# Performance work log

Hardware: AMD Instinct MI355X
Metric: run time of the kernel (lower is better)

## Reference

```python
import jax, jax.numpy as jnp
import numpy as np

DECAY = 0.999
EPS = 1e-05
COMMIT = 0.25


def _layer_norm(x, g, b, eps=1e-5):
    mu = x.mean(-1, keepdims=True)
    var = ((x - mu) ** 2).mean(-1, keepdims=True)
    return (x - mu) * jax.lax.rsqrt(var + eps) * g + b


def setup_inputs() -> dict:
    key = jax.random.key(0)
    ks = jax.random.split(key, 8)
    B, T, D, M, H = 8, 4096, 512, 1024, 512
    init_bound = 1.0 / 512
    embedding = jax.random.uniform(ks[0], (M, D), jnp.float32, -init_bound, init_bound)
    return {
        "dense_x": jax.random.normal(ks[1], (B, T, D), jnp.float32),
        "dense_padding_mask": jax.random.randint(ks[2], (B, T), 0, 2).astype(bool),
        "labels": jax.random.randint(ks[3], (B, T), 0, M),
        "embedding": embedding,
        "ema_count": jnp.zeros((M,), jnp.float32),
        "ema_weight": embedding,
        "ln1_g": jnp.ones((D,), jnp.float32),
        "ln1_b": jnp.zeros((D,), jnp.float32),
        "W1": jax.random.normal(ks[4], (D, H), jnp.float32) * (1.0 / np.sqrt(D)),
        "ln2_g": jnp.ones((H,), jnp.float32),
        "ln2_b": jnp.zeros((H,), jnp.float32),
        "W2": jax.random.normal(ks[5], (H, M), jnp.float32) * (1.0 / np.sqrt(H)),
    }


def reference(dense_x, dense_padding_mask, labels, embedding, ema_count, ema_weight,
              ln1_g, ln1_b, W1, ln2_g, ln2_b, W2):
    B, T, D = dense_x.shape
    M = embedding.shape[0]
    N = B * T

    # ---- VQ codebook (EMA) ----
    x_flat = jax.lax.stop_gradient(dense_x).reshape(N, D)
    distances = (jnp.sum(embedding ** 2, axis=1)[None, :]
                 + jnp.sum(x_flat ** 2, axis=1, keepdims=True)
                 - 2.0 * (x_flat @ embedding.T))
    indices = jnp.argmin(distances, axis=-1)  # [N]
    quantized = embedding[indices].reshape(B, T, D)

    # EMA codebook update (training path); encodings.sum(0) and encodings.T @ x
    # expressed as scatter-adds instead of materializing [N, M] one-hot.
    counts = jnp.zeros((M,), dense_x.dtype).at[indices].add(1.0)
    new_count = DECAY * ema_count + (1.0 - DECAY) * counts
    n = jnp.sum(new_count)
    new_count = (new_count + EPS) / (n + M * EPS) * n
    dw = jnp.zeros((M, D), dense_x.dtype).at[indices].add(x_flat)
    new_weight = DECAY * ema_weight + (1.0 - DECAY) * dw
    new_embedding = new_weight / new_count[:, None]

    e_latent_loss = (dense_x - jax.lax.stop_gradient(quantized)) ** 2  # [B,T,D]
    vq_loss = COMMIT * e_latent_loss
    quantized_st = dense_x + jax.lax.stop_gradient(quantized - dense_x)

    avg_probs = counts / N
    perplexity = jnp.exp(-jnp.sum(avg_probs * jnp.log(avg_probs + 1e-10)))

    # ---- decoder: LN -> ReLU -> Linear -> LN -> ReLU -> Linear ----
    h = jax.nn.relu(_layer_norm(dense_x, ln1_g, ln1_b)) @ W1      # [B,T,H]
    logits = jax.nn.relu(_layer_norm(h, ln2_g, ln2_b)) @ W2       # [B,T,M]

    # ---- cross-entropy with ignore_index=-1 (padding) ----
    lab = jnp.where(dense_padding_mask, -1, labels)
    valid = lab >= 0
    safe = jnp.where(valid, lab, 0)
    logp = jax.nn.log_softmax(logits, axis=-1)
    ce = -jnp.take_along_axis(logp, safe[..., None], axis=-1)[..., 0]
    recon_loss = jnp.where(valid, ce, 0.0)

    loss = recon_loss + vq_loss.sum(-1)  # [B,T]
    return quantized_st, loss, perplexity, new_embedding, new_count, new_weight
```

## Files before the change

kernel.cpp:

```cpp
#include <hip/hip_runtime.h>


#define N_TOK 32768
#define WAITV(n) __builtin_amdgcn_s_waitcnt(0x0F70 | (n))
#define BAR() __builtin_amdgcn_s_barrier()

typedef __attribute__((ext_vector_type(8))) short short8;
typedef _Float16 half8 __attribute__((ext_vector_type(8)));
typedef __attribute__((ext_vector_type(4))) float f32x4;

__device__ __forceinline__ f32x4 mfma16(short8 a, short8 b, f32x4 c) {
    return __builtin_amdgcn_mfma_f32_16x16x32_bf16(a, b, c, 0, 0, 0);
}
__device__ __forceinline__ f32x4 mfma16h(half8 a, half8 b, f32x4 c) {
    return __builtin_amdgcn_mfma_f32_16x16x32_f16(a, b, c, 0, 0, 0);
}

__device__ __forceinline__ void gl_lds16(const unsigned short* g, char* l) {
    __builtin_amdgcn_global_load_lds(
        (const __attribute__((address_space(1))) void*)g,
        (__attribute__((address_space(3))) void*)l, 16, 0, 0);
}

__device__ __forceinline__ unsigned short f2bf(float x) {
    unsigned u = __float_as_uint(x);
    u += 0x7fffu + ((u >> 16) & 1u);
    return (unsigned short)(u >> 16);
}
__device__ __forceinline__ float bf2f(unsigned short h) {
    return __uint_as_float(((unsigned)h) << 16);
}
__device__ __forceinline__ unsigned short f2h(float x) {
    union { _Float16 h; unsigned short u; } c;
    c.h = (_Float16)x;
    return c.u;
}
__device__ __forceinline__ float h2f(unsigned short u) {
    union { _Float16 h; unsigned short u; } c;
    c.u = u;
    return (float)c.h;
}

__device__ __forceinline__ float waveSum(float v) {
#pragma unroll
    for (int off = 32; off > 0; off >>= 1) v += __shfl_down(v, off, 64);
    return v;
}
__device__ __forceinline__ float xorSum(float v) {
#pragma unroll
    for (int off = 1; off < 64; off <<= 1) v += __shfl_xor(v, off);
    return v;
}

__global__ __launch_bounds__(256) void prep_x_kernel(
        const float* __restrict__ X, const float* __restrict__ g,
        const float* __restrict__ b, unsigned short* __restrict__ Xf,
        unsigned short* __restrict__ A1, unsigned long long* __restrict__ minpack) {
    int tid = threadIdx.x;
    if (tid < 4) minpack[(blockIdx.x << 2) + tid] = ~0ULL;
    int lane = tid & 63;
    int n = (blockIdx.x << 2) + (tid >> 6);
    const float* row = X + ((size_t)n << 9);
    float v[8]; float s = 0.f, ss = 0.f;
#pragma unroll
    for (int i = 0; i < 8; ++i) { v[i] = row[lane + (i << 6)]; s += v[i]; ss += v[i] * v[i]; }
    s = xorSum(s); ss = xorSum(ss);
    float mu = s * (1.f / 512.f);
    float rs = rsqrtf(ss * (1.f / 512.f) - mu * mu + 1e-5f);
#pragma unroll
    for (int i = 0; i < 8; ++i) {
        int c = lane + (i << 6);
        size_t o = ((size_t)n << 9) + c;
        float x = v[i];
        Xf[o] = f2h(x);
        float a = fmaxf((x - mu) * rs * g[c] + b[c], 0.f);
        A1[o] = f2bf(a);
    }
}

__global__ __launch_bounds__(256) void prep_h_kernel(
        const unsigned short* __restrict__ Hb, const float* __restrict__ g,
        const float* __restrict__ b, unsigned short* __restrict__ A2) {
    int lane = threadIdx.x & 63;
    int n = (blockIdx.x << 2) + (threadIdx.x >> 6);
    const unsigned short* row = Hb + ((size_t)n << 9);
    float v[8]; float s = 0.f, ss = 0.f;
#pragma unroll
    for (int i = 0; i < 8; ++i) { v[i] = bf2f(row[lane + (i << 6)]); s += v[i]; ss += v[i] * v[i]; }
    s = xorSum(s); ss = xorSum(ss);
    float mu = s * (1.f / 512.f);
    float rs = rsqrtf(ss * (1.f / 512.f) - mu * mu + 1e-5f);
#pragma unroll
    for (int i = 0; i < 8; ++i) {
        int c = lane + (i << 6);
        float a = fmaxf((v[i] - mu) * rs * g[c] + b[c], 0.f);
        A2[((size_t)n << 9) + c] = f2bf(a);
    }
}

__global__ __launch_bounds__(256) void prep_e_kernel(
        const float* __restrict__ E, unsigned short* __restrict__ Ehf,
        unsigned short* __restrict__ Elf, float* __restrict__ e_sq,
        int* __restrict__ izero) {
    if (blockIdx.x < 8) izero[(blockIdx.x << 8) + threadIdx.x] = 0;
    int lane = threadIdx.x & 63;
    int m = (blockIdx.x << 2) + (threadIdx.x >> 6);
    const float* row = E + ((size_t)m << 9);
    float ss = 0.f;
#pragma unroll
    for (int i = 0; i < 8; ++i) {
        int c = lane + (i << 6);
        float x = row[c];
        ss += x * x;
        float xs = x * 512.f;
        unsigned short h = f2h(xs);
        size_t o = ((size_t)m << 9) + c;
        Ehf[o] = h;
        Elf[o] = f2h(xs - h2f(h));
    }
    ss = xorSum(ss);
    if (lane == 0) e_sq[m] = ss * 512.f;
}

__global__ __launch_bounds__(256) void prep_wt_kernel(
        const float* __restrict__ W1, const float* __restrict__ W2,
        unsigned short* __restrict__ W1T, unsigned short* __restrict__ W2T) {
    __shared__ float t[32][33];
    int bx = blockIdx.x;
    const float* W = (bx < 16) ? W1 : W2;
    unsigned short* WT = (bx < 16) ? W1T : W2T;
    int Nw = (bx < 16) ? 512 : 1024;
    int n0 = ((bx < 16) ? bx : (bx - 16)) << 5, k0 = blockIdx.y << 5;
    int tx = threadIdx.x & 31, ty = threadIdx.x >> 5;
#pragma unroll
    for (int l = 0; l < 4; ++l)
        t[ty + (l << 3)][tx] = W[(size_t)(k0 + ty + (l << 3)) * Nw + n0 + tx];
    __syncthreads();
#pragma unroll
    for (int l = 0; l < 4; ++l)
        WT[(((size_t)(n0 + ty + (l << 3))) << 9) + k0 + tx] = f2bf(t[tx][ty + (l << 3)]);
}

__device__ __forceinline__ unsigned long long packDist(float d, int m) {
    unsigned u = __float_as_uint(d);
    u = (u & 0x80000000u) ? ~u : (u | 0x80000000u);
    return ((unsigned long long)u << 32) | (unsigned)m;
}

__global__ __launch_bounds__(256) void dist_mfma_kernel(
        const unsigned short* __restrict__ Xf,
        const unsigned short* __restrict__ Ehf, const unsigned short* __restrict__ Elf,
        const float* __restrict__ e_sq, unsigned long long* __restrict__ minpack) {
    __shared__ __align__(16) short L[2][3][4096];
    int tid = threadIdx.x, lane = tid & 63, w = tid >> 6;
    int quad = lane >> 4, lanelo = lane & 15;
    int wm = w >> 1, wn = w & 1;
    int bid = blockIdx.x, xcd = bid & 7, s = bid >> 3;
    int row0 = (((s >> 3) << 3) | xcd) << 7;
    int m0 = (s & 7) << 7;

    int srow = ((w & 1) << 6) + lane;
    int skoff = (w >> 1) << 4;
    const unsigned short* pX = Xf  + (((size_t)(row0 + srow)) << 9) + skoff;
    const unsigned short* pH = Ehf + (((size_t)(m0  + srow)) << 9) + skoff;
    const unsigned short* pL = Elf + (((size_t)(m0  + srow)) << 9) + skoff;
    char* ldsB = (char*)&L[0][0][0] + ((w >> 1) << 12) + ((w & 1) << 10) + (lane << 4);
    const char* ra  = (const char*)&L[0][0][0] + (quad << 11) + (((wm << 6) + lanelo) << 4);
    const char* rbh = (const char*)&L[0][1][0] + (quad << 11) + (((wn << 6) + lanelo) << 4);

    f32x4 acc[4][4];
#pragma unroll
    for (int i = 0; i < 4; ++i)
#pragma unroll
        for (int j = 0; j < 4; ++j) acc[i][j] = 0.f;

    gl_lds16(pX, ldsB);            gl_lds16(pX + 8, ldsB + 2048);
    gl_lds16(pH, ldsB + 8192);     gl_lds16(pH + 8, ldsB + 10240);
    gl_lds16(pL, ldsB + 16384);    gl_lds16(pL + 8, ldsB + 18432);

#pragma unroll
    for (int it = 0; it < 16; ++it) {
        const int cb = it & 1;
        if (it < 15) {
            const unsigned short* sX = pX + ((it + 1) << 5);
            const unsigned short* sH = pH + ((it + 1) << 5);
            const unsigned short* sL = pL + ((it + 1) << 5);
            char* d = ldsB + (cb ^ 1) * 24576;
            gl_lds16(sX, d);           gl_lds16(sX + 8, d + 2048);
            gl_lds16(sH, d + 8192);    gl_lds16(sH + 8, d + 10240);
            gl_lds16(sL, d + 16384);   gl_lds16(sL + 8, d + 18432);
            WAITV(6);
        } else {
            WAITV(0);
        }
        BAR();
        const char* A  = ra  + cb * 24576;
        const char* Bh = rbh + cb * 24576;
        half8 av[4], bh[4], bl[4];
#pragma unroll
        for (int i = 0; i < 4; ++i) av[i] = *(const half8*)(A + (i << 8));
#pragma unroll
        for (int j = 0; j < 4; ++j) {
            bh[j] = *(const half8*)(Bh + (j << 8));
            bl[j] = *(const half8*)(Bh + 8192 + (j << 8));
        }
#pragma unroll
        for (int i = 0; i < 4; ++i)
#pragma unroll
            for (int j = 0; j < 4; ++j) acc[i][j] = mfma16h(av[i], bh[j], acc[i][j]);
#pragma unroll
        for (int i = 0; i < 4; ++i)
#pragma unroll
            for (int j = 0; j < 4; ++j) acc[i][j] = mfma16h(av[i], bl[j], acc[i][j]);
        BAR();
    }

    float esq[4];
#pragma unroll
    for (int j = 0; j < 4; ++j) esq[j] = e_sq[m0 + (wn << 6) + (j << 4) + lanelo];
#pragma unroll
    for (int i = 0; i < 4; ++i)
#pragma unroll
        for (int r = 0; r < 4; ++r) {
            unsigned long long best = ~0ULL;
#pragma unroll
            for (int j = 0; j < 4; ++j) {
                int code = m0 + (wn << 6) + (j << 4) + lanelo;
                float d = esq[j] - 2.f * acc[i][j][r];
                unsigned long long p = packDist(d, code);
                if (p < best) best = p;
            }
#pragma unroll
            for (int off = 1; off < 16; off <<= 1) {
                unsigned long long q = __shfl_xor(best, off);
                if (q < best) best = q;
            }
            if (lanelo == 0) {
                int t = row0 + (wm << 6) + (i << 4) + (quad << 2) + r;
                atomicMin(&minpack[t], best);
            }
        }
}

__global__ __launch_bounds__(256) void gather_kernel(
        const float* __restrict__ X, const float* __restrict__ E,
        const unsigned long long* __restrict__ minpack,
        float* __restrict__ out_q, int* __restrict__ icounts,
        float* __restrict__ vqsum) {
    int lane = threadIdx.x & 63;
    int n = (blockIdx.x << 2) + (threadIdx.x >> 6);
    int idx = (int)(minpack[n] & 0xFFFFFFFFULL);
    if (lane == 0) atomicAdd(&icounts[idx], 1);
    const float* xr = X + ((size_t)n << 9);
    const float* er = E + ((size_t)idx << 9);
    float s = 0.f;
#pragma unroll
    for (int i = 0; i < 8; ++i) {
        int c = lane + (i << 6);
        float xv = xr[c], q = er[c];
        out_q[((size_t)n << 9) + c] = q;
        float dlt = xv - q;
        s += dlt * dlt;
    }
    s = waveSum(s);
    if (lane == 0) vqsum[n] = 0.25f * s;
}

__global__ __launch_bounds__(1024) void codebook_kernel(
        const float* __restrict__ ema_count, const int* __restrict__ icounts,
        float* __restrict__ out_perp, float* __restrict__ out_newcount,
        int* __restrict__ offsets) {
    __shared__ int sc[1024];
    __shared__ float red[16];
    int tid = threadIdx.x;
    int lane = tid & 63, wid = tid >> 6;
    int ic = icounts[tid];
    sc[tid] = ic;
    for (int off = 1; off < 1024; off <<= 1) {
        __syncthreads();
        int v = (tid >= off) ? sc[tid - off] : 0;
        __syncthreads();
        sc[tid] += v;
    }
    offsets[tid] = sc[tid] - ic;
    __syncthreads();

    float cnt = (float)ic;
    float raw = 0.999f * ema_count[tid] + 0.001f * cnt;
    float v = waveSum(raw);
    if (lane == 0) red[wid] = v;
    __syncthreads();
    float nsum = 0.f;
#pragma unroll
    for (int i = 0; i < 16; ++i) nsum += red[i];
    __syncthreads();
    float p = cnt * (1.f / 32768.f);
    float e = p * logf(p + 1e-10f);
    e = waveSum(e);
    if (lane == 0) red[wid] = e;
    __syncthreads();
    float ent = 0.f;
#pragma unroll
    for (int i = 0; i < 16; ++i) ent += red[i];
    float nc = (raw + 1e-5f) / (nsum + 1024.f * 1e-5f) * nsum;
    out_newcount[tid] = nc;
    if (tid == 0) out_perp[0] = expf(-ent);
}

__global__ __launch_bounds__(256) void scatter_kernel(
        const unsigned long long* __restrict__ minpack,
        const int* __restrict__ offsets, int* __restrict__ cursor,
        int* __restrict__ bucket) {
    int n = (blockIdx.x << 8) + threadIdx.x;
    int idx = (int)(minpack[n] & 0xFFFFFFFFULL);
    int pos = atomicAdd(&cursor[idx], 1);
    bucket[offsets[idx] + pos] = n;
}

__global__ __launch_bounds__(256) void dw_kernel(
        const float* __restrict__ X, const int* __restrict__ bucket,
        const int* __restrict__ icounts, const int* __restrict__ offsets,
        float* __restrict__ dw) {
    __shared__ float comb[4][512];
    int tid = threadIdx.x, lane = tid & 63, w = tid >> 6;
    int m = blockIdx.x;
    int cnt = icounts[m], base = offsets[m];
    float acc[8] = {};
    for (int i = w; i < cnt; i += 4) {
        int t = bucket[base + i];
        const float* xr = X + ((size_t)t << 9);
#pragma unroll
        for (int j = 0; j < 8; ++j) acc[j] += xr[lane + (j << 6)];
    }
#pragma unroll
    for (int j = 0; j < 8; ++j) comb[w][lane + (j << 6)] = acc[j];
    __syncthreads();
    for (int c = tid; c < 512; c += 256)
        dw[((size_t)m << 9) + c] = comb[0][c] + comb[1][c] + comb[2][c] + comb[3][c];
}

__global__ __launch_bounds__(256) void gemm1_mfma_kernel(
        const unsigned short* __restrict__ A1, const unsigned short* __restrict__ W1T,
        unsigned short* __restrict__ Hb) {
    __shared__ __align__(16) short L[2][2][4096];
    int tid = threadIdx.x, lane = tid & 63, w = tid >> 6;
    int quad = lane >> 4, lanelo = lane & 15;
    int wm = w >> 1, wn = w & 1;
    int bid = blockIdx.x, xcd = bid & 7, s = bid >> 3;
    int row0 = (((s >> 2) << 3) | xcd) << 7;
    int n0 = (s & 3) << 7;

    int srow = ((w & 1) << 6) + lane;
    int skoff = (w >> 1) << 4;
    const unsigned short* pA = A1  + (((size_t)(row0 + srow)) << 9) + skoff;
    const unsigned short* pB = W1T + (((size_t)(n0   + srow)) << 9) + skoff;
    char* ldsB = (char*)&L[0][0][0] + ((w >> 1) << 12) + ((w & 1) << 10) + (lane << 4);
    const char* ra = (const char*)&L[0][0][0] + (quad << 11) + (((wm << 6) + lanelo) << 4);
    const char* rb = (const char*)&L[0][1][0] + (quad << 11) + (((wn << 6) + lanelo) << 4);

    f32x4 acc[4][4];
#pragma unroll
    for (int i = 0; i < 4; ++i)
#pragma unroll
        for (int j = 0; j < 4; ++j) acc[i][j] = 0.f;

    gl_lds16(pA, ldsB);          gl_lds16(pA + 8, ldsB + 2048);
    gl_lds16(pB, ldsB + 8192);   gl_lds16(pB + 8, ldsB + 10240);

#pragma unroll
    for (int it = 0; it < 16; ++it) {
        const int cb = it & 1;
        if (it < 15) {
            const unsigned short* sA = pA + ((it + 1) << 5);
            const unsigned short* sB = pB + ((it + 1) << 5);
            char* d = ldsB + (cb ^ 1) * 16384;
            gl_lds16(sA, d);          gl_lds16(sA + 8, d + 2048);
            gl_lds16(sB, d + 8192);   gl_lds16(sB + 8, d + 10240);
            WAITV(4);
        } else {
            WAITV(0);
        }
        BAR();
        const char* A = ra + cb * 16384;
        const char* B = rb + cb * 16384;
        short8 af[4], bf4[4];
#pragma unroll
        for (int i = 0; i < 4; ++i) af[i] = *(const short8*)(A + (i << 8));
#pragma unroll
        for (int j = 0; j < 4; ++j) bf4[j] = *(const short8*)(B + (j << 8));
#pragma unroll
        for (int i = 0; i < 4; ++i)
#pragma unroll
            for (int j = 0; j < 4; ++j) acc[i][j] = mfma16(af[i], bf4[j], acc[i][j]);
        BAR();
    }
#pragma unroll
    for (int i = 0; i < 4; ++i)
#pragma unroll
        for (int j = 0; j < 4; ++j)
#pragma unroll
            for (int r = 0; r < 4; ++r) {
                int row = row0 + (wm << 6) + (i << 4) + (quad << 2) + r;
                int col = n0 + (wn << 6) + (j << 4) + lanelo;
                Hb[((size_t)row << 9) + col] = f2bf(acc[i][j][r]);
            }
}

__global__ __launch_bounds__(256) void gemm2_chunk_kernel(
        const unsigned short* __restrict__ A2, const unsigned short* __restrict__ W2T,
        const int* __restrict__ mask, const int* __restrict__ labels,
        float* __restrict__ ws_cmax, float* __restrict__ ws_csum,
        float* __restrict__ ws_lab) {
    __shared__ __align__(16) short L[2][2][4096];
    __shared__ float lmax[2][2][64], lsum[2][2][64], llab[128];
    __shared__ int slab[128];
    int tid = threadIdx.x, lane = tid & 63, w = tid >> 6;
    int quad = lane >> 4, lanelo = lane & 15;
    int wm = w >> 1, wn = w & 1;
    int bid = blockIdx.x, xcd = bid & 7, s = bid >> 3;
    int row0 = (((s >> 3) << 3) | xcd) << 7;
    int cy = s & 7;
    int c0 = cy << 7;
    if (tid < 128) {
        int mk = mask[row0 + tid];
        slab[tid] = mk ? 0 : labels[row0 + tid];
    }
    __syncthreads();

    int srow = ((w & 1) << 6) + lane;
    int skoff = (w >> 1) << 4;
    const unsigned short* pA = A2  + (((size_t)(row0 + srow)) << 9) + skoff;
    const unsigned short* pB = W2T + (((size_t)(c0   + srow)) << 9) + skoff;
    char* ldsB = (char*)&L[0][0][0] + ((w >> 1) << 12) + ((w & 1) << 10) + (lane << 4);
    const char* ra = (const char*)&L[0][0][0] + (quad << 11) + (((wm << 6) + lanelo) << 4);
    const char* rb = (const char*)&L[0][1][0] + (quad << 11) + (((wn << 6) + lanelo) << 4);

    f32x4 acc[4][4];
#pragma unroll
    for (int i = 0; i < 4; ++i)
#pragma unroll
        for (int j = 0; j < 4; ++j) acc[i][j] = 0.f;

    gl_lds16(pA, ldsB);          gl_lds16(pA + 8, ldsB + 2048);
    gl_lds16(pB, ldsB + 8192);   gl_lds16(pB + 8, ldsB + 10240);

#pragma unroll
    for (int it = 0; it < 16; ++it) {
        const int cb = it & 1;
        if (it < 15) {
            const unsigned short* sA = pA + ((it + 1) << 5);
            const unsigned short* sB = pB + ((it + 1) << 5);
            char* d = ldsB + (cb ^ 1) * 16384;
            gl_lds16(sA, d);          gl_lds16(sA + 8, d + 2048);
            gl_lds16(sB, d + 8192);   gl_lds16(sB + 8, d + 10240);
            WAITV(4);
        } else {
            WAITV(0);
        }
        BAR();
        const char* A = ra + cb * 16384;
        const char* B = rb + cb * 16384;
        short8 af[4], bf4[4];
#pragma unroll
        for (int i = 0; i < 4; ++i) af[i] = *(const short8*)(A + (i << 8));
#pragma unroll
        for (int j = 0; j < 4; ++j) bf4[j] = *(const short8*)(B + (j << 8));
#pragma unroll
        for (int i = 0; i < 4; ++i)
#pragma unroll
            for (int j = 0; j < 4; ++j) acc[i][j] = mfma16(af[i], bf4[j], acc[i][j]);
        BAR();
    }

#pragma unroll
    for (int i = 0; i < 4; ++i)
#pragma unroll
        for (int j = 0; j < 4; ++j)
#pragma unroll
            for (int r = 0; r < 4; ++r) {
                int code = c0 + (wn << 6) + (j << 4) + lanelo;
                int tt = (wm << 6) + (i << 4) + (quad << 2) + r;
                if (code == slab[tt]) llab[tt] = acc[i][j][r];
            }
#pragma unroll
    for (int i = 0; i < 4; ++i)
#pragma unroll
        for (int r = 0; r < 4; ++r) {
            float mx = fmaxf(fmaxf(acc[i][0][r], acc[i][1][r]),
                             fmaxf(acc[i][2][r], acc[i][3][r]));
#pragma unroll
            for (int off = 1; off < 16; off <<= 1) mx = fmaxf(mx, __shfl_xor(mx, off));
            if (lanelo == 0) lmax[wm][wn][(i << 4) + (quad << 2) + r] = mx;
        }
    __syncthreads();
#pragma unroll
    for (int i = 0; i < 4; ++i)
#pragma unroll
        for (int r = 0; r < 4; ++r) {
            int tl = (i << 4) + (quad << 2) + r;
            float cm = fmaxf(lmax[wm][0][tl], lmax[wm][1][tl]);
            float s2 = expf(acc[i][0][r] - cm) + expf(acc[i][1][r] - cm) +
                       expf(acc[i][2][r] - cm) + expf(acc[i][3][r] - cm);
#pragma unroll
            for (int off = 1; off < 16; off <<= 1) s2 += __shfl_xor(s2, off);
            if (lanelo == 0) lsum[wm][wn][tl] = s2;
        }
    __syncthreads();
    if (tid < 128) {
        int wmi = tid >> 6, tl = tid & 63;
        int token = row0 + tid;
        float cm = fmaxf(lmax[wmi][0][tl], lmax[wmi][1][tl]);
        float cs = lsum[wmi][0][tl] + lsum[wmi][1][tl];
        size_t o = ((size_t)cy << 15) + token;
        ws_cmax[o] = cm;
        ws_csum[o] = cs;
        if ((slab[tid] >> 7) == cy) ws_lab[token] = llab[tid];
    }
}

__global__ __launch_bounds__(256) void epilogue_kernel(
        const float* __restrict__ ema_weight, const float* __restrict__ dw,
        const float* __restrict__ newcount, float* __restrict__ out_neww,
        float* __restrict__ out_newemb,
        const float* __restrict__ ws_cmax, const float* __restrict__ ws_csum,
        const float* __restrict__ ws_lab, const int* __restrict__ mask,
        const float* __restrict__ vqsum, float* __restrict__ loss_out) {
    int bx = blockIdx.x;
    if (bx < 2048) {
        int i = (bx << 8) + threadIdx.x;
        float nw = 0.999f * ema_weight[i] + 0.001f * dw[i];
        out_neww[i] = nw;
        out_newemb[i] = nw / newcount[i >> 9];
    } else {
        int n = ((bx - 2048) << 8) + threadIdx.x;
        float m[8], s[8];
#pragma unroll
        for (int c = 0; c < 8; ++c) {
            m[c] = ws_cmax[(c << 15) + n];
            s[c] = ws_csum[(c << 15) + n];
        }
        float gm = m[0];
#pragma unroll
        for (int c = 1; c < 8; ++c) gm = fmaxf(gm, m[c]);
        float se = 0.f;
#pragma unroll
        for (int c = 0; c < 8; ++c) se += s[c] * expf(m[c] - gm);
        float ce = -(ws_lab[n] - gm - logf(se));
        loss_out[n] = (mask[n] ? 0.f : ce) + vqsum[n];
    }
}

extern "C" void kernel_launch(void* const* d_in, const int* in_sizes, int n_in,
                              void* d_out, int out_size, void* d_ws, size_t ws_size,
                              hipStream_t stream) {
    const float* X          = (const float*)d_in[0];
    const int*   mask       = (const int*)d_in[1];
    const int*   labels     = (const int*)d_in[2];
    const float* E          = (const float*)d_in[3];
    const float* ema_count  = (const float*)d_in[4];
    const float* ema_weight = (const float*)d_in[5];
    const float* g1 = (const float*)d_in[6];
    const float* b1 = (const float*)d_in[7];
    const float* W1 = (const float*)d_in[8];
    const float* g2 = (const float*)d_in[9];
    const float* b2 = (const float*)d_in[10];
    const float* W2 = (const float*)d_in[11];

    float* out = (float*)d_out;
    float* out_q        = out;
    float* out_loss     = out + 16777216;
    float* out_perp     = out + 16809984;
    float* out_newemb   = out + 16809985;
    float* out_newcount = out + 17334273;
    float* out_neww     = out + 17335297;

    float* w = (float*)d_ws;
    float* vqsum = w;  w += 32768;
    float* e_sq = w;   w += 1024;
    float* dwbuf = w;  w += 524288;
    unsigned long long* minpack = (unsigned long long*)w; w += 65536;
    float* ws_cmax = w; w += 262144;
    float* ws_csum = w; w += 262144;
    float* ws_lab  = w; w += 32768;
    int* icounts = (int*)w; w += 1024;
    int* cursor  = (int*)w; w += 1024;
    int* offsets = (int*)w; w += 1024;
    int* bucket  = (int*)w; w += 32768;
    unsigned short* Ehf = (unsigned short*)w; w += 262144;
    unsigned short* Elf = (unsigned short*)w; w += 262144;
    unsigned short* W1T = (unsigned short*)w; w += 131072;
    unsigned short* W2T = (unsigned short*)w; w += 262144;
    unsigned short* Xf  = (unsigned short*)w; w += 8388608;
    unsigned short* A1  = (unsigned short*)w; w += 8388608;
    unsigned short* Hb  = (unsigned short*)w; w += 8388608;
    unsigned short* A2  = Xf;

    prep_e_kernel<<<256, 256, 0, stream>>>(E, Ehf, Elf, e_sq, icounts);
    prep_wt_kernel<<<dim3(48, 16), 256, 0, stream>>>(W1, W2, W1T, W2T);
    prep_x_kernel<<<8192, 256, 0, stream>>>(X, g1, b1, Xf, A1, minpack);
    dist_mfma_kernel<<<2048, 256, 0, stream>>>(Xf, Ehf, Elf, e_sq, minpack);
    gather_kernel<<<8192, 256, 0, stream>>>(X, E, minpack, out_q, icounts, vqsum);
    codebook_kernel<<<1, 1024, 0, stream>>>(ema_count, icounts, out_perp,
                                            out_newcount, offsets);
    scatter_kernel<<<128, 256, 0, stream>>>(minpack, offsets, cursor, bucket);
    dw_kernel<<<1024, 256, 0, stream>>>(X, bucket, icounts, offsets, dwbuf);
    gemm1_mfma_kernel<<<1024, 256, 0, stream>>>(A1, W1T, Hb);
    prep_h_kernel<<<8192, 256, 0, stream>>>(Hb, g2, b2, A2);
    gemm2_chunk_kernel<<<2048, 256, 0, stream>>>(A2, W2T, mask, labels,
                                                 ws_cmax, ws_csum, ws_lab);
    epilogue_kernel<<<2176, 256, 0, stream>>>(ema_weight, dwbuf, out_newcount,
                                              out_neww, out_newemb,
                                              ws_cmax, ws_csum, ws_lab,
                                              mask, vqsum, out_loss);
}
```

Baseline: 475.7 us.

## Enlarge MFMA GEMM tiles to 256 rows per block in distance and decoder GEMMs

The distance, gemm1 and gemm2 kernels now compute 256x128 output tiles per block instead of 128x128. Each wave holds 8x4 accumulators, and the A and B LDS staging layouts are redone, with gemm1 and gemm2 sharing a new gemm_core helper. The grid sizes are halved to match. This doubles B-operand reuse and cuts global and LDS traffic per FLOP, at the cost of more registers and LDS per block, which may lower occupancy.

Result: slower. 600.2 us (+26.2%).

```diff
diff --git a/kernel.cpp b/kernel.cpp
--- a/kernel.cpp
+++ b/kernel.cpp
@@ -151,65 +151,70 @@
         const unsigned short* __restrict__ Xf,
         const unsigned short* __restrict__ Ehf, const unsigned short* __restrict__ Elf,
         const float* __restrict__ e_sq, unsigned long long* __restrict__ minpack) {
-    __shared__ __align__(16) short L[2][3][4096];
+    __shared__ __align__(16) char LB[65536];
     int tid = threadIdx.x, lane = tid & 63, w = tid >> 6;
     int quad = lane >> 4, lanelo = lane & 15;
     int wm = w >> 1, wn = w & 1;
-    int bid = blockIdx.x, xcd = bid & 7, s = bid >> 3;
-    int row0 = (((s >> 3) << 3) | xcd) << 7;
+    int bid = blockIdx.x, x = bid & 7, s = bid >> 3;
+    int row0 = (((s >> 3) << 3) | x) << 8;
     int m0 = (s & 7) << 7;
 
-    int srow = ((w & 1) << 6) + lane;
-    int skoff = (w >> 1) << 4;
-    const unsigned short* pX = Xf  + (((size_t)(row0 + srow)) << 9) + skoff;
-    const unsigned short* pH = Ehf + (((size_t)(m0  + srow)) << 9) + skoff;
-    const unsigned short* pL = Elf + (((size_t)(m0  + srow)) << 9) + skoff;
-    char* ldsB = (char*)&L[0][0][0] + ((w >> 1) << 12) + ((w & 1) << 10) + (lane << 4);
-    const char* ra  = (const char*)&L[0][0][0] + (quad << 11) + (((wm << 6) + lanelo) << 4);
-    const char* rbh = (const char*)&L[0][1][0] + (quad << 11) + (((wn << 6) + lanelo) << 4);
-
-    f32x4 acc[4][4];
-#pragma unroll
-    for (int i = 0; i < 4; ++i)
+    const unsigned short* pA = Xf  + (((size_t)(row0 + tid)) << 9);
+    int nB = tid & 127, kB0 = (tid >> 7) << 1;
+    const unsigned short* pH = Ehf + (((size_t)(m0 + nB)) << 9) + (kB0 << 3);
+    const unsigned short* pL = Elf + (((size_t)(m0 + nB)) << 9) + (kB0 << 3);
+    char* dA  = LB + (tid << 4);
+    char* dBh = LB + 16384 + (kB0 << 11) + (nB << 4);
+    char* dBl = dBh + 8192;
+    const char* ra  = LB + (quad << 12) + (((wm << 7) + lanelo) << 4);
+    const char* rbh = LB + 16384 + (quad << 11) + (((wn << 6) + lanelo) << 4);
+
+    f32x4 acc[8][4];
+#pragma unroll
+    for (int i = 0; i < 8; ++i)
 #pragma unroll
         for (int j = 0; j < 4; ++j) acc[i][j] = 0.f;
 
-    gl_lds16(pX, ldsB);            gl_lds16(pX + 8, ldsB + 2048);
-    gl_lds16(pH, ldsB + 8192);     gl_lds16(pH + 8, ldsB + 10240);
-    gl_lds16(pL, ldsB + 16384);    gl_lds16(pL + 8, ldsB + 18432);
+    gl_lds16(pA, dA);            gl_lds16(pA + 8, dA + 4096);
+    gl_lds16(pA + 16, dA + 8192); gl_lds16(pA + 24, dA + 12288);
+    gl_lds16(pH, dBh);           gl_lds16(pH + 8, dBh + 2048);
+    gl_lds16(pL, dBl);           gl_lds16(pL + 8, dBl + 2048);
 
 #pragma unroll
     for (int it = 0; it < 16; ++it) {
         const int cb = it & 1;
         if (it < 15) {
-            const unsigned short* sX = pX + ((it + 1) << 5);
+            const unsigned short* sA = pA + ((it + 1) << 5);
             const unsigned short* sH = pH + ((it + 1) << 5);
             const unsigned short* sL = pL + ((it + 1) << 5);
-            char* d = ldsB + (cb ^ 1) * 24576;
-            gl_lds16(sX, d);           gl_lds16(sX + 8, d + 2048);
-            gl_lds16(sH, d + 8192);    gl_lds16(sH + 8, d + 10240);
-            gl_lds16(sL, d + 16384);   gl_lds16(sL + 8, d + 18432);
-            WAITV(6);
+            char* eA  = dA  + (cb ^ 1) * 32768;
+            char* eBh = dBh + (cb ^ 1) * 32768;
+            char* eBl = dBl + (cb ^ 1) * 32768;
+            gl_lds16(sA, eA);            gl_lds16(sA + 8, eA + 4096);
+            gl_lds16(sA + 16, eA + 8192); gl_lds16(sA + 24, eA + 12288);
+            gl_lds16(sH, eBh);           gl_lds16(sH + 8, eBh + 2048);
+            gl_lds16(sL, eBl);           gl_lds16(sL + 8, eBl + 2048);
+            WAITV(8);
         } else {
             WAITV(0);
         }
         BAR();
-        const char* A  = ra  + cb * 24576;
-        const char* Bh = rbh + cb * 24576;
-        half8 av[4], bh[4], bl[4];
-#pragma unroll
-        for (int i = 0; i < 4; ++i) av[i] = *(const half8*)(A + (i << 8));
+        const char* A  = ra  + cb * 32768;
+        const char* Bh = rbh + cb * 32768;
+        half8 av[8], bh[4], bl[4];
+#pragma unroll
+        for (int i = 0; i < 8; ++i) av[i] = *(const half8*)(A + (i << 8));
 #pragma unroll
         for (int j = 0; j < 4; ++j) {
             bh[j] = *(const half8*)(Bh + (j << 8));
             bl[j] = *(const half8*)(Bh + 8192 + (j << 8));
         }
 #pragma unroll
-        for (int i = 0; i < 4; ++i)
+        for (int i = 0; i < 8; ++i)
 #pragma unroll
             for (int j = 0; j < 4; ++j) acc[i][j] = mfma16h(av[i], bh[j], acc[i][j]);
 #pragma unroll
-        for (int i = 0; i < 4; ++i)
+        for (int i = 0; i < 8; ++i)
 #pragma unroll
             for (int j = 0; j < 4; ++j) acc[i][j] = mfma16h(av[i], bl[j], acc[i][j]);
         BAR();
@@ -219,7 +224,7 @@
 #pragma unroll
     for (int j = 0; j < 4; ++j) esq[j] = e_sq[m0 + (wn << 6) + (j << 4) + lanelo];
 #pragma unroll
-    for (int i = 0; i < 4; ++i)
+    for (int i = 0; i < 8; ++i)
 #pragma unroll
         for (int r = 0; r < 4; ++r) {
             unsigned long long best = ~0ULL;
@@ -232,14 +237,176 @@
             }
 #pragma unroll
             for (int off = 1; off < 16; off <<= 1) {
-                unsigned long long q = __shfl_xor(best, off);
-                if (q < best) best = q;
+                unsigned long long q2 = __shfl_xor(best, off);
+                if (q2 < best) best = q2;
             }
             if (lanelo == 0) {
-                int t = row0 + (wm << 6) + (i << 4) + (quad << 2) + r;
+                int t = row0 + (wm << 7) + (i << 4) + (quad << 2) + r;
                 atomicMin(&minpack[t], best);
             }
         }
+}
+
+__device__ __forceinline__ void gemm_core(
+        char* LB, const unsigned short* pA, const unsigned short* pB,
+        char* dBbase, f32x4 (*acc)[4]) {
+    int tid = threadIdx.x, lane = tid & 63, w = tid >> 6;
+    int quad = lane >> 4, lanelo = lane & 15;
+    int wm = w >> 1, wn = w & 1;
+    char* dA = LB + (tid << 4);
+    char* dB = dBbase;
+    const char* ra = LB + (quad << 12) + (((wm << 7) + lanelo) << 4);
+    const char* rb = LB + 16384 + (quad << 11) + (((wn << 6) + lanelo) << 4);
+
+    gl_lds16(pA, dA);            gl_lds16(pA + 8, dA + 4096);
+    gl_lds16(pA + 16, dA + 8192); gl_lds16(pA + 24, dA + 12288);
+    gl_lds16(pB, dB);            gl_lds16(pB + 8, dB + 2048);
+
+#pragma unroll
+    for (int it = 0; it < 16; ++it) {
+        const int cb = it & 1;
+        if (it < 15) {
+            const unsigned short* sA = pA + ((it + 1) << 5);
+            const unsigned short* sB = pB + ((it + 1) << 5);
+            char* eA = dA + (cb ^ 1) * 24576;
+            char* eB = dB + (cb ^ 1) * 24576;
+            gl_lds16(sA, eA);            gl_lds16(sA + 8, eA + 4096);
+            gl_lds16(sA + 16, eA + 8192); gl_lds16(sA + 24, eA + 12288);
+            gl_lds16(sB, eB);            gl_lds16(sB + 8, eB + 2048);
+            WAITV(6);
+        } else {
+            WAITV(0);
+        }
+        BAR();
+        const char* A = ra + cb * 24576;
+        const char* B = rb + cb * 24576;
+        short8 af[8], bf4[4];
+#pragma unroll
+        for (int i = 0; i < 8; ++i) af[i] = *(const short8*)(A + (i << 8));
+#pragma unroll
+        for (int j = 0; j < 4; ++j) bf4[j] = *(const short8*)(B + (j << 8));
+#pragma unroll
+        for (int i = 0; i < 8; ++i)
+#pragma unroll
+            for (int j = 0; j < 4; ++j) acc[i][j] = mfma16(af[i], bf4[j], acc[i][j]);
+        BAR();
+    }
+}
+
+__global__ __launch_bounds__(256) void gemm1_mfma_kernel(
+        const unsigned short* __restrict__ A1, const unsigned short* __restrict__ W1T,
+        unsigned short* __restrict__ Hb) {
+    __shared__ __align__(16) char LB[49152];
+    int tid = threadIdx.x, lane = tid & 63, w = tid >> 6;
+    int quad = lane >> 4, lanelo = lane & 15;
+    int wm = w >> 1, wn = w & 1;
+    int bid = blockIdx.x, x = bid & 7, s = bid >> 3;
+    int row0 = (((s >> 2) << 3) | x) << 8;
+    int n0 = (s & 3) << 7;
+
+    const unsigned short* pA = A1 + (((size_t)(row0 + tid)) << 9);
+    int nB = tid & 127, kB0 = (tid >> 7) << 1;
+    const unsigned short* pB = W1T + (((size_t)(n0 + nB)) << 9) + (kB0 << 3);
+    char* dB = LB + 16384 + (kB0 << 11) + (nB << 4);
+
+    f32x4 acc[8][4];
+#pragma unroll
+    for (int i = 0; i < 8; ++i)
+#pragma unroll
+        for (int j = 0; j < 4; ++j) acc[i][j] = 0.f;
+
+    gemm_core(LB, pA, pB, dB, acc);
+
+#pragma unroll
+    for (int i = 0; i < 8; ++i)
+#pragma unroll
+        for (int j = 0; j < 4; ++j)
+#pragma unroll
+            for (int r = 0; r < 4; ++r) {
+                int row = row0 + (wm << 7) + (i << 4) + (quad << 2) + r;
+                int col = n0 + (wn << 6) + (j << 4) + lanelo;
+                Hb[((size_t)row << 9) + col] = f2bf(acc[i][j][r]);
+            }
+}
+
+__global__ __launch_bounds__(256) void gemm2_chunk_kernel(
+        const unsigned short* __restrict__ A2, const unsigned short* __restrict__ W2T,
+        const int* __restrict__ mask, const int* __restrict__ labels,
+        float* __restrict__ ws_cmax, float* __restrict__ ws_csum,
+        float* __restrict__ ws_lab) {
+    __shared__ __align__(16) char LB[49152];
+    __shared__ float lmax[2][2][128], lsum[2][2][128], llab[256];
+    __shared__ int slab[256];
+    int tid = threadIdx.x, lane = tid & 63, w = tid >> 6;
+    int quad = lane >> 4, lanelo = lane & 15;
+    int wm = w >> 1, wn = w & 1;
+    int bid = blockIdx.x, x = bid & 7, s = bid >> 3;
+    int row0 = (((s >> 3) << 3) | x) << 8;
+    int cy = s & 7;
+    int c0 = cy << 7;
+    {
+        int mk = mask[row0 + tid];
+        slab[tid] = mk ? 0 : labels[row0 + tid];
+    }
+    __syncthreads();
+
+    const unsigned short* pA = A2 + (((size_t)(row0 + tid)) << 9);
+    int nB = tid & 127, kB0 = (tid >> 7) << 1;
+    const unsigned short* pB = W2T + (((size_t)(c0 + nB)) << 9) + (kB0 << 3);
+    char* dB = LB + 16384 + (kB0 << 11) + (nB << 4);
+
+    f32x4 acc[8][4];
+#pragma unroll
+    for (int i = 0; i < 8; ++i)
+#pragma unroll
+        for (int j = 0; j < 4; ++j) acc[i][j] = 0.f;
+
+    gemm_core(LB, pA, pB, dB, acc);
+
+#pragma unroll
+    for (int i = 0; i < 8; ++i)
+#pragma unroll
+        for (int j = 0; j < 4; ++j)
+#pragma unroll
+            for (int r = 0; r < 4; ++r) {
+                int code = c0 + (wn << 6) + (j << 4) + lanelo;
+                int tt = (wm << 7) + (i << 4) + (quad << 2) + r;
+                if (code == slab[tt]) llab[tt] = acc[i][j][r];
+            }
+#pragma unroll
+    for (int i = 0; i < 8; ++i)
+#pragma unroll
+        for (int r = 0; r < 4; ++r) {
+            float mx = fmaxf(fmaxf(acc[i][0][r], acc[i][1][r]),
+                             fmaxf(acc[i][2][r], acc[i][3][r]));
+#pragma unroll
+            for (int off = 1; off < 16; off <<= 1) mx = fmaxf(mx, __shfl_xor(mx, off));
+            if (lanelo == 0) lmax[wm][wn][(i << 4) + (quad << 2) + r] = mx;
+        }
+    __syncthreads();
+#pragma unroll
+    for (int i = 0; i < 8; ++i)
+#pragma unroll
+        for (int r = 0; r < 4; ++r) {
+            int tl = (i << 4) + (quad << 2) + r;
+            float cm = fmaxf(lmax[wm][0][tl], lmax[wm][1][tl]);
+            float s2 = expf(acc[i][0][r] - cm) + expf(acc[i][1][r] - cm) +
+                       expf(acc[i][2][r] - cm) + expf(acc[i][3][r] - cm);
+#pragma unroll
+            for (int off = 1; off < 16; off <<= 1) s2 += __shfl_xor(s2, off);
+            if (lanelo == 0) lsum[wm][wn][tl] = s2;
+        }
+    __syncthreads();
+    {
+        int wmi = tid >> 7, tl = tid & 127;
+        int token = row0 + tid;
+        float cm = fmaxf(lmax[wmi][0][tl], lmax[wmi][1][tl]);
+        float cs = lsum[wmi][0][tl] + lsum[wmi][1][tl];
+        size_t o = ((size_t)cy << 15) + token;
+        ws_cmax[o] = cm;
+        ws_csum[o] = cs;
+        if ((slab[tid] >> 7) == cy) ws_lab[token] = llab[tid];
+    }
 }
 
 __global__ __launch_bounds__(256) void gather_kernel(
@@ -337,185 +504,6 @@
     __syncthreads();
     for (int c = tid; c < 512; c += 256)
         dw[((size_t)m << 9) + c] = comb[0][c] + comb[1][c] + comb[2][c] + comb[3][c];
-}
-
-__global__ __launch_bounds__(256) void gemm1_mfma_kernel(
-        const unsigned short* __restrict__ A1, const unsigned short* __restrict__ W1T,
-        unsigned short* __restrict__ Hb) {
-    __shared__ __align__(16) short L[2][2][4096];
-    int tid = threadIdx.x, lane = tid & 63, w = tid >> 6;
-    int quad = lane >> 4, lanelo = lane & 15;
-    int wm = w >> 1, wn = w & 1;
-    int bid = blockIdx.x, xcd = bid & 7, s = bid >> 3;
-    int row0 = (((s >> 2) << 3) | xcd) << 7;
-    int n0 = (s & 3) << 7;
-
-    int srow = ((w & 1) << 6) + lane;
-    int skoff = (w >> 1) << 4;
-    const unsigned short* pA = A1  + (((size_t)(row0 + srow)) << 9) + skoff;
-    const unsigned short* pB = W1T + (((size_t)(n0   + srow)) << 9) + skoff;
-    char* ldsB = (char*)&L[0][0][0] + ((w >> 1) << 12) + ((w & 1) << 10) + (lane << 4);
-    const char* ra = (const char*)&L[0][0][0] + (quad << 11) + (((wm << 6) + lanelo) << 4);
-    const char* rb = (const char*)&L[0][1][0] + (quad << 11) + (((wn << 6) + lanelo) << 4);
-
-    f32x4 acc[4][4];
-#pragma unroll
-    for (int i = 0; i < 4; ++i)
-#pragma unroll
-        for (int j = 0; j < 4; ++j) acc[i][j] = 0.f;
-
-    gl_lds16(pA, ldsB);          gl_lds16(pA + 8, ldsB + 2048);
-    gl_lds16(pB, ldsB + 8192);   gl_lds16(pB + 8, ldsB + 10240);
-
-#pragma unroll
-    for (int it = 0; it < 16; ++it) {
-        const int cb = it & 1;
-        if (it < 15) {
-            const unsigned short* sA = pA + ((it + 1) << 5);
-            const unsigned short* sB = pB + ((it + 1) << 5);
-            char* d = ldsB + (cb ^ 1) * 16384;
-            gl_lds16(sA, d);          gl_lds16(sA + 8, d + 2048);
-            gl_lds16(sB, d + 8192);   gl_lds16(sB + 8, d + 10240);
-            WAITV(4);
-        } else {
-            WAITV(0);
-        }
-        BAR();
-        const char* A = ra + cb * 16384;
-        const char* B = rb + cb * 16384;
-        short8 af[4], bf4[4];
-#pragma unroll
-        for (int i = 0; i < 4; ++i) af[i] = *(const short8*)(A + (i << 8));
-#pragma unroll
-        for (int j = 0; j < 4; ++j) bf4[j] = *(const short8*)(B + (j << 8));
-#pragma unroll
-        for (int i = 0; i < 4; ++i)
-#pragma unroll
-            for (int j = 0; j < 4; ++j) acc[i][j] = mfma16(af[i], bf4[j], acc[i][j]);
-        BAR();
-    }
-#pragma unroll
-    for (int i = 0; i < 4; ++i)
-#pragma unroll
-        for (int j = 0; j < 4; ++j)
-#pragma unroll
-            for (int r = 0; r < 4; ++r) {
-                int row = row0 + (wm << 6) + (i << 4) + (quad << 2) + r;
-                int col = n0 + (wn << 6) + (j << 4) + lanelo;
-                Hb[((size_t)row << 9) + col] = f2bf(acc[i][j][r]);
-            }
-}
-
-__global__ __launch_bounds__(256) void gemm2_chunk_kernel(
-        const unsigned short* __restrict__ A2, const unsigned short* __restrict__ W2T,
-        const int* __restrict__ mask, const int* __restrict__ labels,
-        float* __restrict__ ws_cmax, float* __restrict__ ws_csum,
-        float* __restrict__ ws_lab) {
-    __shared__ __align__(16) short L[2][2][4096];
-    __shared__ float lmax[2][2][64], lsum[2][2][64], llab[128];
-    __shared__ int slab[128];
-    int tid = threadIdx.x, lane = tid & 63, w = tid >> 6;
-    int quad = lane >> 4, lanelo = lane & 15;
-    int wm = w >> 1, wn = w & 1;
-    int bid = blockIdx.x, xcd = bid & 7, s = bid >> 3;
-    int row0 = (((s >> 3) << 3) | xcd) << 7;
-    int cy = s & 7;
-    int c0 = cy << 7;
-    if (tid < 128) {
-        int mk = mask[row0 + tid];
-        slab[tid] = mk ? 0 : labels[row0 + tid];
-    }
-    __syncthreads();
-
-    int srow = ((w & 1) << 6) + lane;
-    int skoff = (w >> 1) << 4;
-    const unsigned short* pA = A2  + (((size_t)(row0 + srow)) << 9) + skoff;
-    const unsigned short* pB = W2T + (((size_t)(c0   + srow)) << 9) + skoff;
-    char* ldsB = (char*)&L[0][0][0] + ((w >> 1) << 12) + ((w & 1) << 10) + (lane << 4);
-    const char* ra = (const char*)&L[0][0][0] + (quad << 11) + (((wm << 6) + lanelo) << 4);
-    const char* rb = (const char*)&L[0][1][0] + (quad << 11) + (((wn << 6) + lanelo) << 4);
-
-    f32x4 acc[4][4];
-#pragma unroll
-    for (int i = 0; i < 4; ++i)
-#pragma unroll
-        for (int j = 0; j < 4; ++j) acc[i][j] = 0.f;
-
-    gl_lds16(pA, ldsB);          gl_lds16(pA + 8, ldsB + 2048);
-    gl_lds16(pB, ldsB + 8192);   gl_lds16(pB + 8, ldsB + 10240);
-
-#pragma unroll
-    for (int it = 0; it < 16; ++it) {
-        const int cb = it & 1;
-        if (it < 15) {
-            const unsigned short* sA = pA + ((it + 1) << 5);
-            const unsigned short* sB = pB + ((it + 1) << 5);
-            char* d = ldsB + (cb ^ 1) * 16384;
-            gl_lds16(sA, d);          gl_lds16(sA + 8, d + 2048);
-            gl_lds16(sB, d + 8192);   gl_lds16(sB + 8, d + 10240);
-            WAITV(4);
-        } else {
-            WAITV(0);
-        }
-        BAR();
-        const char* A = ra + cb * 16384;
-        const char* B = rb + cb * 16384;
-        short8 af[4], bf4[4];
-#pragma unroll
-        for (int i = 0; i < 4; ++i) af[i] = *(const short8*)(A + (i << 8));
-#pragma unroll
-        for (int j = 0; j < 4; ++j) bf4[j] = *(const short8*)(B + (j << 8));
-#pragma unroll
-        for (int i = 0; i < 4; ++i)
-#pragma unroll
-            for (int j = 0; j < 4; ++j) acc[i][j] = mfma16(af[i], bf4[j], acc[i][j]);
-        BAR();
-    }
-
-#pragma unroll
-    for (int i = 0; i < 4; ++i)
-#pragma unroll
-        for (int j = 0; j < 4; ++j)
-#pragma unroll
-            for (int r = 0; r < 4; ++r) {
-                int code = c0 + (wn << 6) + (j << 4) + lanelo;
-                int tt = (wm << 6) + (i << 4) + (quad << 2) + r;
-                if (code == slab[tt]) llab[tt] = acc[i][j][r];
-            }
-#pragma unroll
-    for (int i = 0; i < 4; ++i)
-#pragma unroll
-        for (int r = 0; r < 4; ++r) {
-            float mx = fmaxf(fmaxf(acc[i][0][r], acc[i][1][r]),
-                             fmaxf(acc[i][2][r], acc[i][3][r]));
-#pragma unroll
-            for (int off = 1; off < 16; off <<= 1) mx = fmaxf(mx, __shfl_xor(mx, off));
-            if (lanelo == 0) lmax[wm][wn][(i << 4) + (quad << 2) + r] = mx;
-        }
-    __syncthreads();
-#pragma unroll
-    for (int i = 0; i < 4; ++i)
-#pragma unroll
-        for (int r = 0; r < 4; ++r) {
-            int tl = (i << 4) + (quad << 2) + r;
-            float cm = fmaxf(lmax[wm][0][tl], lmax[wm][1][tl]);
-            float s2 = expf(acc[i][0][r] - cm) + expf(acc[i][1][r] - cm) +
-                       expf(acc[i][2][r] - cm) + expf(acc[i][3][r] - cm);
-#pragma unroll
-            for (int off = 1; off < 16; off <<= 1) s2 += __shfl_xor(s2, off);
-            if (lanelo == 0) lsum[wm][wn][tl] = s2;
-        }
-    __syncthreads();
-    if (tid < 128) {
-        int wmi = tid >> 6, tl = tid & 63;
-        int token = row0 + tid;
-        float cm = fmaxf(lmax[wmi][0][tl], lmax[wmi][1][tl]);
-        float cs = lsum[wmi][0][tl] + lsum[wmi][1][tl];
-        size_t o = ((size_t)cy << 15) + token;
-        ws_cmax[o] = cm;
-        ws_csum[o] = cs;
-        if ((slab[tid] >> 7) == cy) ws_lab[token] = llab[tid];
-    }
 }
 
 __global__ __launch_bounds__(256) void epilogue_kernel(
@@ -598,15 +586,15 @@
     prep_e_kernel<<<256, 256, 0, stream>>>(E, Ehf, Elf, e_sq, icounts);
     prep_wt_kernel<<<dim3(48, 16), 256, 0, stream>>>(W1, W2, W1T, W2T);
     prep_x_kernel<<<8192, 256, 0, stream>>>(X, g1, b1, Xf, A1, minpack);
-    dist_mfma_kernel<<<2048, 256, 0, stream>>>(Xf, Ehf, Elf, e_sq, minpack);
+    dist_mfma_kernel<<<1024, 256, 0, stream>>>(Xf, Ehf, Elf, e_sq, minpack);
     gather_kernel<<<8192, 256, 0, stream>>>(X, E, minpack, out_q, icounts, vqsum);
     codebook_kernel<<<1, 1024, 0, stream>>>(ema_count, icounts, out_perp,
                                             out_newcount, offsets);
     scatter_kernel<<<128, 256, 0, stream>>>(minpack, offsets, cursor, bucket);
     dw_kernel<<<1024, 256, 0, stream>>>(X, bucket, icounts, offsets, dwbuf);
-    gemm1_mfma_kernel<<<1024, 256, 0, stream>>>(A1, W1T, Hb);
+    gemm1_mfma_kernel<<<512, 256, 0, stream>>>(A1, W1T, Hb);
     prep_h_kernel<<<8192, 256, 0, stream>>>(Hb, g2, b2, A2);
-    gemm2_chunk_kernel<<<2048, 256, 0, stream>>>(A2, W2T, mask, labels,
+    gemm2_chunk_kernel<<<1024, 256, 0, stream>>>(A2, W2T, mask, labels,
                                                  ws_cmax, ws_csum, ws_lab);
     epilogue_kernel<<<2176, 256, 0, stream>>>(ema_weight, dwbuf, out_newcount,
                                               out_neww, out_newemb,
```
